# Kernel tuning notes

Measured on AMD Instinct MI355X. Metric: run time of the kernel, lower is better.

Reference implementation:

```python
import jax, jax.numpy as jnp
import numpy as np

T, H, L, OUT = 100, 100, 5, 10  # seq_len, hidden/input dim, n_lstm_layers, output dim


def _lstm_layer(x, Wih, Whh, bih, bhh):
    """Single-layer LSTM, PyTorch gate order (i, f, g, o).
    x: [T, B, H] -> outputs [T, B, H]. Zero initial state."""
    B = x.shape[1]
    b = bih + bhh  # [4H]
    # precompute input contributions for all timesteps: [T, B, 4H]
    xg = jnp.einsum('tbi,gi->tbg', x, Wih) + b

    def step(carry, xg_t):
        h, c = carry
        gates = xg_t + h @ Whh.T  # [B, 4H]
        i, f, g, o = jnp.split(gates, 4, axis=-1)
        i = jax.nn.sigmoid(i)
        f = jax.nn.sigmoid(f)
        g = jnp.tanh(g)
        o = jax.nn.sigmoid(o)
        c = f * c + i * g
        h = o * jnp.tanh(c)
        return (h, c), h

    h0 = jnp.zeros((B, H), dtype=x.dtype)
    c0 = jnp.zeros((B, H), dtype=x.dtype)
    _, ys = jax.lax.scan(step, (h0, c0), xg)
    return ys  # [T, B, H]


def setup_inputs() -> dict:
    key = jax.random.key(0)
    ks = jax.random.split(key, 7)
    s = 0.1
    return {
        'input': jax.random.normal(ks[0], (1, T, H), dtype=jnp.float32),
        'Wih': jax.random.normal(ks[1], (L, 4 * H, H), dtype=jnp.float32) * s,
        'Whh': jax.random.normal(ks[2], (L, 4 * H, H), dtype=jnp.float32) * s,
        'bih': jax.random.normal(ks[3], (L, 4 * H), dtype=jnp.float32) * s,
        'bhh': jax.random.normal(ks[4], (L, 4 * H), dtype=jnp.float32) * s,
        'W_out': jax.random.normal(ks[5], (OUT, H), dtype=jnp.float32) * s,
        'b_out': jax.random.normal(ks[6], (OUT,), dtype=jnp.float32) * s,
    }


def reference(input, Wih, Whh, bih, bhh, W_out, b_out):
    # batch_first [B, T, H] -> time-major [T, B, H] for scan
    x = jnp.transpose(input.reshape(-1, T, H), (1, 0, 2))
    for l in range(L):
        x = _lstm_layer(x, Wih[l], Whh[l], bih[l], bhh[l])
        if l < L - 1:
            x = jax.nn.relu(x)  # inter-layer ReLU (not after last LSTM)
    out = jax.nn.sigmoid(x @ W_out.T + b_out)  # [T, B, OUT]
    return jnp.transpose(out, (1, 0, 2)).reshape(T, OUT)
```

## Files before the change

kernel.cpp:

```cpp
#include <hip/hip_runtime.h>

#define TT 100
#define HH 100
#define NL 5
#define NOUT 10
#define NG 400
#define CC 10
#define NC (TT / CC)

typedef float v2f __attribute__((ext_vector_type(2)));

__device__ __forceinline__ float sigm(float x) { return 1.f / (1.f + __expf(-x)); }

#define RPT25(M) M(0) M(1) M(2) M(3) M(4) M(5) M(6) M(7) M(8) M(9) M(10) M(11) \
                 M(12) M(13) M(14) M(15) M(16) M(17) M(18) M(19) M(20) M(21) M(22) M(23) M(24)

__launch_bounds__(512, 2)
__global__ void lstm_pipe_kernel(
    const float* __restrict__ input,
    const float* __restrict__ Wih,
    const float* __restrict__ Whh,
    const float* __restrict__ bih,
    const float* __restrict__ bhh,
    const float* __restrict__ Wout,
    const float* __restrict__ bout,
    float* __restrict__ out,
    int* __restrict__ flags,
    float* __restrict__ xstage)
{
  const int l = blockIdx.x;
  const int tid = threadIdx.x;
  const int j = tid >> 2;
  const int g = tid & 3;
  const int row = g * HH + j;

  __shared__ __align__(16) float xch[CC * HH];
  __shared__ __align__(16) float och[CC * HH];
  __shared__ __align__(16) float hbuf[2][HH];

#define DECLW(k) v2f wA##k, wB##k, uA##k, uB##k;
  RPT25(DECLW)
  float bias = 0.f;
  if (tid < NG) {
    const float4* wr = (const float4*)(Wih + (size_t)l * NG * HH + (size_t)row * HH);
    const float4* ur = (const float4*)(Whh + (size_t)l * NG * HH + (size_t)row * HH);
#define LOADW(k)                                                         \
  {                                                                      \
    float4 t0 = wr[k];                                                   \
    wA##k = (v2f){t0.x, t0.y}; wB##k = (v2f){t0.z, t0.w};                \
    float4 t1 = ur[k];                                                   \
    uA##k = (v2f){t1.x, t1.y}; uB##k = (v2f){t1.z, t1.w};                \
  }
    RPT25(LOADW)
    bias = bih[l * NG + row] + bhh[l * NG + row];
  }

  float c = 0.f;
  if (tid < HH) hbuf[0][tid] = 0.f;

  for (int ch = 0; ch < NC; ++ch) {
    if (l == 0) {
      if (tid < CC * HH / 4)
        ((float4*)xch)[tid] = ((const float4*)(input + ch * CC * HH))[tid];
    } else {
      if (tid == 0) {
        const int* fl = flags + (l - 1) * NC + ch;
        while (__hip_atomic_load(fl, __ATOMIC_ACQUIRE, __HIP_MEMORY_SCOPE_AGENT) == 0)
          __builtin_amdgcn_s_sleep(1);
      }
      __syncthreads();
      const float4* src =
          (const float4*)(xstage + ((size_t)(l - 1) * TT + (size_t)ch * CC) * HH);
      if (tid < CC * HH / 4) ((float4*)xch)[tid] = src[tid];
    }

#pragma unroll 2
    for (int s = 0; s < CC; ++s) {
      __syncthreads();
      if (tid < NG) {
        const float4* h4 = (const float4*)hbuf[s & 1];
        const float4* x4 = (const float4*)(xch + s * HH);
        v2f p0 = {bias, 0.f}, p1 = {0.f, 0.f}, p2 = {0.f, 0.f}, p3 = {0.f, 0.f};
        v2f q0 = {0.f, 0.f}, q1 = {0.f, 0.f}, q2 = {0.f, 0.f}, q3 = {0.f, 0.f};
#define FMAK(k)                                                             \
  {                                                                         \
    float4 hv = h4[k];                                                      \
    float4 xv = x4[k];                                                      \
    if ((k) & 1) {                                                          \
      p0 = uA##k * (v2f){hv.x, hv.y} + p0;                                  \
      p1 = uB##k * (v2f){hv.z, hv.w} + p1;                                  \
      p2 = wA##k * (v2f){xv.x, xv.y} + p2;                                  \
      p3 = wB##k * (v2f){xv.z, xv.w} + p3;                                  \
    } else {                                                                \
      q0 = uA##k * (v2f){hv.x, hv.y} + q0;                                  \
      q1 = uB##k * (v2f){hv.z, hv.w} + q1;                                  \
      q2 = wA##k * (v2f){xv.x, xv.y} + q2;                                  \
      q3 = wB##k * (v2f){xv.z, xv.w} + q3;                                  \
    }                                                                       \
  }
        RPT25(FMAK)
        v2f tsum = ((p0 + p1) + (p2 + p3)) + ((q0 + q1) + (q2 + q3));
        float a = tsum.x + tsum.y;

        bool isg = (g == 2);
        float m = isg ? 2.f : 1.f;
        float sg = 1.f / (1.f + __expf(-m * a));
        float v = isg ? 2.f * sg - 1.f : sg;

        float v1 = __shfl_xor(v, 1);
        float v2v = __shfl_xor(v, 2);
        float v3 = __shfl_xor(v1, 2);
        if (g == 0) {
          c = v1 * c + v * v2v;
          float tc = 2.f / (1.f + __expf(-2.f * c)) - 1.f;
          float h = v3 * tc;
          hbuf[(s + 1) & 1][j] = h;
          och[s * HH + j] = (l < NL - 1) ? fmaxf(h, 0.f) : h;
        }
      }
    }
    __syncthreads();

    if (l < NL - 1) {
      float4* dst = (float4*)(xstage + ((size_t)l * TT + (size_t)ch * CC) * HH);
      if (tid < CC * HH / 4) dst[tid] = ((const float4*)och)[tid];
      __syncthreads();
      if (tid == 0) {
        __threadfence();
        __hip_atomic_store(flags + l * NC + ch, 1, __ATOMIC_RELEASE,
                           __HIP_MEMORY_SCOPE_AGENT);
      }
    } else {
      if (tid < NG) {
        int p = tid >> 2, q = tid & 3;
        int s2 = p / 10, r = p % 10;
        const float* wrow = Wout + r * HH + q * 25;
        const float* hrow = och + s2 * HH + q * 25;
        float acc = 0.f;
#pragma unroll
        for (int m2 = 0; m2 < 25; ++m2) acc = fmaf(wrow[m2], hrow[m2], acc);
        acc += __shfl_xor(acc, 1);
        acc += __shfl_xor(acc, 2);
        if (q == 0) out[(ch * CC + s2) * NOUT + r] = sigm(acc + bout[r]);
      }
    }
  }
}

extern "C" void kernel_launch(void* const* d_in, const int* in_sizes, int n_in,
                              void* d_out, int out_size, void* d_ws, size_t ws_size,
                              hipStream_t stream) {
  const float* input = (const float*)d_in[0];
  const float* Wih   = (const float*)d_in[1];
  const float* Whh   = (const float*)d_in[2];
  const float* bih   = (const float*)d_in[3];
  const float* bhh   = (const float*)d_in[4];
  const float* Wout  = (const float*)d_in[5];
  const float* bout  = (const float*)d_in[6];
  float* out = (float*)d_out;

  int* flags = (int*)d_ws;
  float* xstage = (float*)((char*)d_ws + 2048);

  hipMemsetAsync(d_ws, 0, 2048, stream);

  lstm_pipe_kernel<<<dim3(NL), dim3(512), 0, stream>>>(
      input, Wih, Whh, bih, bhh, Wout, bout, out, flags, xstage);
}
```

Before: 207.6 us.

## Switch LSTM recurrence to fp16 dot2 with pre-packed weights streamed from memory

Adds a pre-pass kernel that converts Wih/Whh to packed fp16 in a gate-interleaved layout. The recurrent kernel now streams these weights from global memory/L2 each step instead of holding them in registers, and computes gates with v_dot2_f32_f16. Activations, hidden state and the inter-layer staging buffer are also stored as fp16. This halves the FMA instruction count and the staging traffic, but each step now reloads weights from cache instead of registers, adds an extra kernel launch, and loses precision in h, x and the weights.

```diff
diff --git a/kernel.cpp b/kernel.cpp
--- a/kernel.cpp
+++ b/kernel.cpp
@@ -7,61 +7,99 @@
 #define NG 400
 #define CC 10
 #define NC (TT / CC)
-
-typedef float v2f __attribute__((ext_vector_type(2)));
+#define KC 13
+#define KH 104
+
+typedef _Float16 h2f __attribute__((ext_vector_type(2)));
 
 __device__ __forceinline__ float sigm(float x) { return 1.f / (1.f + __expf(-x)); }
 
-#define RPT25(M) M(0) M(1) M(2) M(3) M(4) M(5) M(6) M(7) M(8) M(9) M(10) M(11) \
-                 M(12) M(13) M(14) M(15) M(16) M(17) M(18) M(19) M(20) M(21) M(22) M(23) M(24)
+__device__ __forceinline__ float fdot2u(unsigned a, unsigned b, float c) {
+#if __has_builtin(__builtin_amdgcn_fdot2)
+  return __builtin_amdgcn_fdot2(__builtin_bit_cast(h2f, a),
+                                __builtin_bit_cast(h2f, b), c, false);
+#else
+  float d;
+  asm("v_dot2_f32_f16 %0, %1, %2, %3" : "=v"(d) : "v"(a), "v"(b), "v"(c));
+  return d;
+#endif
+}
+
+__device__ __forceinline__ unsigned pk16(float lo, float hi) {
+  _Float16 l = (_Float16)lo, h = (_Float16)hi;
+  return (unsigned)__builtin_bit_cast(unsigned short, l) |
+         ((unsigned)__builtin_bit_cast(unsigned short, h) << 16);
+}
+
+__global__ void pack_w(const float* __restrict__ Wih, const float* __restrict__ Whh,
+                       uint4* __restrict__ wil, uint4* __restrict__ whl) {
+  const int b = blockIdx.x;
+  const int l = b / KC, m = b % KC;
+  const int tid = threadIdx.x;
+  if (tid >= NG) return;
+  const int row = (tid & 3) * HH + (tid >> 2);
+  const float* sh = Whh + ((size_t)l * NG + row) * HH;
+  const float* si = Wih + ((size_t)l * NG + row) * HH;
+  float4 ha, hb4, ia, ib;
+  if (m < 12) {
+    ha = *(const float4*)(sh + 8 * m); hb4 = *(const float4*)(sh + 8 * m + 4);
+    ia = *(const float4*)(si + 8 * m); ib = *(const float4*)(si + 8 * m + 4);
+  } else {
+    ha = *(const float4*)(sh + 96); hb4 = make_float4(0.f, 0.f, 0.f, 0.f);
+    ia = *(const float4*)(si + 96); ib = make_float4(0.f, 0.f, 0.f, 0.f);
+  }
+  uint4 uh, ui;
+  uh.x = pk16(ha.x, ha.y); uh.y = pk16(ha.z, ha.w);
+  uh.z = pk16(hb4.x, hb4.y); uh.w = pk16(hb4.z, hb4.w);
+  ui.x = pk16(ia.x, ia.y); ui.y = pk16(ia.z, ia.w);
+  ui.z = pk16(ib.x, ib.y); ui.w = pk16(ib.z, ib.w);
+  whl[(size_t)b * NG + tid] = uh;
+  wil[(size_t)b * NG + tid] = ui;
+}
 
 __launch_bounds__(512, 2)
 __global__ void lstm_pipe_kernel(
     const float* __restrict__ input,
-    const float* __restrict__ Wih,
-    const float* __restrict__ Whh,
     const float* __restrict__ bih,
     const float* __restrict__ bhh,
     const float* __restrict__ Wout,
     const float* __restrict__ bout,
     float* __restrict__ out,
     int* __restrict__ flags,
-    float* __restrict__ xstage)
+    unsigned short* __restrict__ xst,
+    const uint4* __restrict__ whl,
+    const uint4* __restrict__ wil)
 {
+  __shared__ __align__(16) unsigned short xh[CC * KH];
+  __shared__ __align__(16) unsigned short hb[2 * KH];
+  __shared__ __align__(16) unsigned short och16[CC * KH];
+  __shared__ __align__(16) float ochf[CC * HH];
+
   const int l = blockIdx.x;
   const int tid = threadIdx.x;
   const int j = tid >> 2;
   const int g = tid & 3;
-  const int row = g * HH + j;
-
-  __shared__ __align__(16) float xch[CC * HH];
-  __shared__ __align__(16) float och[CC * HH];
-  __shared__ __align__(16) float hbuf[2][HH];
-
-#define DECLW(k) v2f wA##k, wB##k, uA##k, uB##k;
-  RPT25(DECLW)
-  float bias = 0.f;
-  if (tid < NG) {
-    const float4* wr = (const float4*)(Wih + (size_t)l * NG * HH + (size_t)row * HH);
-    const float4* ur = (const float4*)(Whh + (size_t)l * NG * HH + (size_t)row * HH);
-#define LOADW(k)                                                         \
-  {                                                                      \
-    float4 t0 = wr[k];                                                   \
-    wA##k = (v2f){t0.x, t0.y}; wB##k = (v2f){t0.z, t0.w};                \
-    float4 t1 = ur[k];                                                   \
-    uA##k = (v2f){t1.x, t1.y}; uB##k = (v2f){t1.z, t1.w};                \
-  }
-    RPT25(LOADW)
-    bias = bih[l * NG + row] + bhh[l * NG + row];
-  }
-
+  const bool act = (tid < NG);
+  const int row = act ? (g * HH + j) : 0;
+
+  const uint4* wh0 = whl + (size_t)l * KC * NG + tid;
+  const uint4* wi0 = wil + (size_t)l * KC * NG + tid;
+  const float bias = bih[l * NG + row] + bhh[l * NG + row];
+
+  if (tid < KH) { hb[tid] = 0; hb[KH + tid] = 0; }
+  if (tid < CC) {
+    *(uint2*)(xh + tid * KH + HH) = make_uint2(0u, 0u);
+    *(uint2*)(och16 + tid * KH + HH) = make_uint2(0u, 0u);
+  }
   float c = 0.f;
-  if (tid < HH) hbuf[0][tid] = 0.f;
 
   for (int ch = 0; ch < NC; ++ch) {
     if (l == 0) {
-      if (tid < CC * HH / 4)
-        ((float4*)xch)[tid] = ((const float4*)(input + ch * CC * HH))[tid];
+      if (tid < 250) {
+        float4 v = ((const float4*)(input + ch * CC * HH))[tid];
+        int s = tid / 25, q = tid % 25;
+        *(uint2*)(xh + s * KH + q * 4) = make_uint2(pk16(v.x, v.y), pk16(v.z, v.w));
+      }
     } else {
       if (tid == 0) {
         const int* fl = flags + (l - 1) * NC + ch;
@@ -69,61 +107,62 @@
           __builtin_amdgcn_s_sleep(1);
       }
       __syncthreads();
-      const float4* src =
-          (const float4*)(xstage + ((size_t)(l - 1) * TT + (size_t)ch * CC) * HH);
-      if (tid < CC * HH / 4) ((float4*)xch)[tid] = src[tid];
+      const uint4* src =
+          (const uint4*)(xst + ((size_t)(l - 1) * TT + (size_t)ch * CC) * KH);
+      if (tid < 130) ((uint4*)xh)[tid] = src[tid];
     }
 
+#define DOT(m)                                                       \
+  {                                                                  \
+    uint4 hv = hb4[m];                                               \
+    uint4 xv = xp4[m];                                               \
+    uint4 uw = wh0[(m)*NG];                                          \
+    uint4 vw = wi0[(m)*NG];                                          \
+    a0 = fdot2u(uw.x, hv.x, a0); a1 = fdot2u(uw.y, hv.y, a1);        \
+    a2 = fdot2u(uw.z, hv.z, a2); a3 = fdot2u(uw.w, hv.w, a3);        \
+    b0 = fdot2u(vw.x, xv.x, b0); b1 = fdot2u(vw.y, xv.y, b1);        \
+    b2 = fdot2u(vw.z, xv.z, b2); b3 = fdot2u(vw.w, xv.w, b3);        \
+  }
 #pragma unroll 2
     for (int s = 0; s < CC; ++s) {
       __syncthreads();
-      if (tid < NG) {
-        const float4* h4 = (const float4*)hbuf[s & 1];
-        const float4* x4 = (const float4*)(xch + s * HH);
-        v2f p0 = {bias, 0.f}, p1 = {0.f, 0.f}, p2 = {0.f, 0.f}, p3 = {0.f, 0.f};
-        v2f q0 = {0.f, 0.f}, q1 = {0.f, 0.f}, q2 = {0.f, 0.f}, q3 = {0.f, 0.f};
-#define FMAK(k)                                                             \
-  {                                                                         \
-    float4 hv = h4[k];                                                      \
-    float4 xv = x4[k];                                                      \
-    if ((k) & 1) {                                                          \
-      p0 = uA##k * (v2f){hv.x, hv.y} + p0;                                  \
-      p1 = uB##k * (v2f){hv.z, hv.w} + p1;                                  \
-      p2 = wA##k * (v2f){xv.x, xv.y} + p2;                                  \
-      p3 = wB##k * (v2f){xv.z, xv.w} + p3;                                  \
-    } else {                                                                \
-      q0 = uA##k * (v2f){hv.x, hv.y} + q0;                                  \
-      q1 = uB##k * (v2f){hv.z, hv.w} + q1;                                  \
-      q2 = wA##k * (v2f){xv.x, xv.y} + q2;                                  \
-      q3 = wB##k * (v2f){xv.z, xv.w} + q3;                                  \
-    }                                                                       \
-  }
-        RPT25(FMAK)
-        v2f tsum = ((p0 + p1) + (p2 + p3)) + ((q0 + q1) + (q2 + q3));
-        float a = tsum.x + tsum.y;
+      if (act) {
+        const uint4* hb4 = (const uint4*)(hb + (s & 1) * KH);
+        const uint4* xp4 = (const uint4*)(xh + s * KH);
+        float a0 = 0.f, a1 = 0.f, a2 = 0.f, a3 = 0.f;
+        float b0 = 0.f, b1 = 0.f, b2 = 0.f, b3 = 0.f;
+        DOT(0) DOT(1) DOT(2) DOT(3) DOT(4) DOT(5) DOT(6)
+        DOT(7) DOT(8) DOT(9) DOT(10) DOT(11) DOT(12)
+        float aa = ((a0 + a1) + (a2 + a3)) + ((b0 + b1) + (b2 + b3)) + bias;
 
         bool isg = (g == 2);
-        float m = isg ? 2.f : 1.f;
-        float sg = 1.f / (1.f + __expf(-m * a));
-        float v = isg ? 2.f * sg - 1.f : sg;
-
-        float v1 = __shfl_xor(v, 1);
-        float v2v = __shfl_xor(v, 2);
+        float mm = isg ? 2.f : 1.f;
+        float sg = 1.f / (1.f + __expf(-mm * aa));
+        float vv = isg ? 2.f * sg - 1.f : sg;
+
+        float v1 = __shfl_xor(vv, 1);
+        float v2v = __shfl_xor(vv, 2);
         float v3 = __shfl_xor(v1, 2);
         if (g == 0) {
-          c = v1 * c + v * v2v;
+          c = v1 * c + vv * v2v;
           float tc = 2.f / (1.f + __expf(-2.f * c)) - 1.f;
           float h = v3 * tc;
-          hbuf[(s + 1) & 1][j] = h;
-          och[s * HH + j] = (l < NL - 1) ? fmaxf(h, 0.f) : h;
+          hb[((s + 1) & 1) * KH + j] =
+              __builtin_bit_cast(unsigned short, (_Float16)h);
+          if (l < NL - 1) {
+            och16[s * KH + j] =
+                __builtin_bit_cast(unsigned short, (_Float16)fmaxf(h, 0.f));
+          } else {
+            ochf[s * HH + j] = h;
+          }
         }
       }
     }
     __syncthreads();
 
     if (l < NL - 1) {
-      float4* dst = (float4*)(xstage + ((size_t)l * TT + (size_t)ch * CC) * HH);
-      if (tid < CC * HH / 4) dst[tid] = ((const float4*)och)[tid];
+      uint4* dst = (uint4*)(xst + ((size_t)l * TT + (size_t)ch * CC) * KH);
+      if (tid < 130) dst[tid] = ((const uint4*)och16)[tid];
       __syncthreads();
       if (tid == 0) {
         __threadfence();
@@ -135,7 +174,7 @@
         int p = tid >> 2, q = tid & 3;
         int s2 = p / 10, r = p % 10;
         const float* wrow = Wout + r * HH + q * 25;
-        const float* hrow = och + s2 * HH + q * 25;
+        const float* hrow = ochf + s2 * HH + q * 25;
         float acc = 0.f;
 #pragma unroll
         for (int m2 = 0; m2 < 25; ++m2) acc = fmaf(wrow[m2], hrow[m2], acc);
@@ -160,10 +199,14 @@
   float* out = (float*)d_out;
 
   int* flags = (int*)d_ws;
-  float* xstage = (float*)((char*)d_ws + 2048);
+  unsigned short* xst = (unsigned short*)((char*)d_ws + 2048);
+  uint4* whl = (uint4*)((char*)d_ws + 85248);
+  uint4* wil = (uint4*)((char*)d_ws + 501248);
 
   hipMemsetAsync(d_ws, 0, 2048, stream);
 
+  pack_w<<<dim3(NL * KC), dim3(512), 0, stream>>>(Wih, Whh, wil, whl);
+
   lstm_pipe_kernel<<<dim3(NL), dim3(512), 0, stream>>>(
-      input, Wih, Whh, bih, bhh, Wout, bout, out, flags, xstage);
-}
+      input, bih, bhh, Wout, bout, out, flags, xst, whl, wil);
+}
```

Result: slower. 296.5 us (+42.8%).

## Switch LSTM recurrence to fp16 dot2 with weights held in AGPRs

Applied to the files above, without the earlier changes.

Weights are converted to packed fp16 and kept in accumulation registers. Each thread now computes all four gates for one hidden unit over a quarter of the reduction dimension, using v_dot2_f32_f16 and a DPP quad reduction in place of per-gate threads and shuffles. Inter-layer activations are staged as fp16 in a padded layout, and a separate pre-kernel packs the input for layer 0. This targets fewer instructions and less LDS/global traffic on the serial per-step path, at the cost of reduced precision in the weights and hidden state plus an extra kernel launch.

```diff
diff --git a/kernel.cpp b/kernel.cpp
--- a/kernel.cpp
+++ b/kernel.cpp
@@ -4,20 +4,64 @@
 #define HH 100
 #define NL 5
 #define NOUT 10
-#define NG 400
 #define CC 10
 #define NC (TT / CC)
-
-typedef float v2f __attribute__((ext_vector_type(2)));
+#define RW 64
+#define NTH 448
+
+typedef _Float16 h2f __attribute__((ext_vector_type(2)));
 
 __device__ __forceinline__ float sigm(float x) { return 1.f / (1.f + __expf(-x)); }
 
-#define RPT25(M) M(0) M(1) M(2) M(3) M(4) M(5) M(6) M(7) M(8) M(9) M(10) M(11) \
-                 M(12) M(13) M(14) M(15) M(16) M(17) M(18) M(19) M(20) M(21) M(22) M(23) M(24)
-
-__launch_bounds__(512, 2)
-__global__ void lstm_pipe_kernel(
-    const float* __restrict__ input,
+__device__ __forceinline__ float fdot2u(unsigned a, unsigned b, float c) {
+#if __has_builtin(__builtin_amdgcn_fdot2)
+  return __builtin_amdgcn_fdot2(__builtin_bit_cast(h2f, a),
+                                __builtin_bit_cast(h2f, b), c, false);
+#else
+  float d;
+  asm("v_dot2_f32_f16 %0, %1, %2, %3" : "=v"(d) : "v"(a), "v"(b), "v"(c));
+  return d;
+#endif
+}
+
+__device__ __forceinline__ unsigned pk16(float lo, float hi) {
+  _Float16 l = (_Float16)lo, h = (_Float16)hi;
+  return (unsigned)__builtin_bit_cast(unsigned short, l) |
+         ((unsigned)__builtin_bit_cast(unsigned short, h) << 16);
+}
+
+__device__ __forceinline__ float qred(float p) {
+  int t = __builtin_amdgcn_update_dpp(0, __builtin_bit_cast(int, p), 0xB1, 0xF,
+                                      0xF, true);
+  p += __builtin_bit_cast(float, t);
+  t = __builtin_amdgcn_update_dpp(0, __builtin_bit_cast(int, p), 0x4E, 0xF, 0xF,
+                                  true);
+  p += __builtin_bit_cast(float, t);
+  return p;
+}
+
+#define R13(M) M(0) M(1) M(2) M(3) M(4) M(5) M(6) M(7) M(8) M(9) M(10) M(11) M(12)
+
+#define AWR(D, S) asm volatile("v_accvgpr_write_b32 %0, %1" : "=a"(D) : "v"(S));
+#define ARD(D, S) asm("v_accvgpr_read_b32 %0, %1" : "=v"(D) : "a"(S));
+
+__global__ void pack_x0(const float* __restrict__ in, unsigned* __restrict__ x0) {
+  for (int idx = blockIdx.x * 512 + threadIdx.x; idx < TT * RW;
+       idx += gridDim.x * 512) {
+    int t = idx / RW, d = idx & (RW - 1);
+    int q = d >> 4, m = d & 15;
+    unsigned v = 0u;
+    int k0 = 26 * q + 2 * m;
+    if (m < 13 && k0 < 100) {
+      v = pk16(in[t * HH + k0], in[t * HH + k0 + 1]);
+    }
+    x0[idx] = v;
+  }
+}
+
+__global__ __attribute__((amdgpu_flat_work_group_size(NTH, NTH),
+                          amdgpu_waves_per_eu(2, 2)))
+void lstm_pipe_kernel(
     const float* __restrict__ Wih,
     const float* __restrict__ Whh,
     const float* __restrict__ bih,
@@ -26,104 +70,152 @@
     const float* __restrict__ bout,
     float* __restrict__ out,
     int* __restrict__ flags,
-    float* __restrict__ xstage)
+    unsigned* __restrict__ xst)
 {
+  __shared__ __align__(16) unsigned xh32[CC * RW];
+  __shared__ __align__(16) unsigned och32[CC * RW];
+  __shared__ __align__(16) unsigned hb32[2 * RW];
+  __shared__ __align__(16) float ochf[CC * HH];
+
   const int l = blockIdx.x;
   const int tid = threadIdx.x;
   const int j = tid >> 2;
-  const int g = tid & 3;
-  const int row = g * HH + j;
-
-  __shared__ __align__(16) float xch[CC * HH];
-  __shared__ __align__(16) float och[CC * HH];
-  __shared__ __align__(16) float hbuf[2][HH];
-
-#define DECLW(k) v2f wA##k, wB##k, uA##k, uB##k;
-  RPT25(DECLW)
-  float bias = 0.f;
-  if (tid < NG) {
-    const float4* wr = (const float4*)(Wih + (size_t)l * NG * HH + (size_t)row * HH);
-    const float4* ur = (const float4*)(Whh + (size_t)l * NG * HH + (size_t)row * HH);
-#define LOADW(k)                                                         \
-  {                                                                      \
-    float4 t0 = wr[k];                                                   \
-    wA##k = (v2f){t0.x, t0.y}; wB##k = (v2f){t0.z, t0.w};                \
-    float4 t1 = ur[k];                                                   \
-    uA##k = (v2f){t1.x, t1.y}; uB##k = (v2f){t1.z, t1.w};                \
+  const int q = tid & 3;
+  const bool act = (tid < 400);
+  const int hwpos = (j / 26) * 32 + (j % 26);
+
+#define DECLM(m) unsigned H0_##m, H1_##m, H2_##m, H3_##m, \
+                          I0_##m, I1_##m, I2_##m, I3_##m;
+  R13(DECLM)
+
+  float b0 = 0.f, b1 = 0.f, b2 = 0.f, b3 = 0.f;
+  if (act) {
+    const int kq = 26 * q;
+    const float* ph0 = Whh + (size_t)(l * 400 + 0 * 100 + j) * 100 + kq;
+    const float* ph1 = Whh + (size_t)(l * 400 + 1 * 100 + j) * 100 + kq;
+    const float* ph2 = Whh + (size_t)(l * 400 + 2 * 100 + j) * 100 + kq;
+    const float* ph3 = Whh + (size_t)(l * 400 + 3 * 100 + j) * 100 + kq;
+    const float* pi0 = Wih + (size_t)(l * 400 + 0 * 100 + j) * 100 + kq;
+    const float* pi1 = Wih + (size_t)(l * 400 + 1 * 100 + j) * 100 + kq;
+    const float* pi2 = Wih + (size_t)(l * 400 + 2 * 100 + j) * 100 + kq;
+    const float* pi3 = Wih + (size_t)(l * 400 + 3 * 100 + j) * 100 + kq;
+#define LDM(m)                                                           \
+    {                                                                    \
+      const bool ok = (kq + 2 * (m)) < 100;                              \
+      float2 f; unsigned u;                                              \
+      f = ok ? *(const float2*)(ph0 + 2 * (m)) : make_float2(0.f, 0.f);  \
+      u = pk16(f.x, f.y); AWR(H0_##m, u)                                 \
+      f = ok ? *(const float2*)(ph1 + 2 * (m)) : make_float2(0.f, 0.f);  \
+      u = pk16(f.x, f.y); AWR(H1_##m, u)                                 \
+      f = ok ? *(const float2*)(ph2 + 2 * (m)) : make_float2(0.f, 0.f);  \
+      u = pk16(f.x, f.y); AWR(H2_##m, u)                                 \
+      f = ok ? *(const float2*)(ph3 + 2 * (m)) : make_float2(0.f, 0.f);  \
+      u = pk16(f.x, f.y); AWR(H3_##m, u)                                 \
+      f = ok ? *(const float2*)(pi0 + 2 * (m)) : make_float2(0.f, 0.f);  \
+      u = pk16(f.x, f.y); AWR(I0_##m, u)                                 \
+      f = ok ? *(const float2*)(pi1 + 2 * (m)) : make_float2(0.f, 0.f);  \
+      u = pk16(f.x, f.y); AWR(I1_##m, u)                                 \
+      f = ok ? *(const float2*)(pi2 + 2 * (m)) : make_float2(0.f, 0.f);  \
+      u = pk16(f.x, f.y); AWR(I2_##m, u)                                 \
+      f = ok ? *(const float2*)(pi3 + 2 * (m)) : make_float2(0.f, 0.f);  \
+      u = pk16(f.x, f.y); AWR(I3_##m, u)                                 \
+    }
+    R13(LDM)
+    if (q == 0) {
+      b0 = bih[l * 400 + 0 * 100 + j] + bhh[l * 400 + 0 * 100 + j];
+      b1 = bih[l * 400 + 1 * 100 + j] + bhh[l * 400 + 1 * 100 + j];
+      b2 = bih[l * 400 + 2 * 100 + j] + bhh[l * 400 + 2 * 100 + j];
+      b3 = bih[l * 400 + 3 * 100 + j] + bhh[l * 400 + 3 * 100 + j];
+    }
   }
-    RPT25(LOADW)
-    bias = bih[l * NG + row] + bhh[l * NG + row];
-  }
-
+
+  if (tid < 2 * RW) hb32[tid] = 0u;
+  if (tid < 160) ((uint4*)och32)[tid] = make_uint4(0u, 0u, 0u, 0u);
   float c = 0.f;
-  if (tid < HH) hbuf[0][tid] = 0.f;
+  __syncthreads();
 
   for (int ch = 0; ch < NC; ++ch) {
-    if (l == 0) {
-      if (tid < CC * HH / 4)
-        ((float4*)xch)[tid] = ((const float4*)(input + ch * CC * HH))[tid];
-    } else {
+    if (l > 0) {
       if (tid == 0) {
         const int* fl = flags + (l - 1) * NC + ch;
         while (__hip_atomic_load(fl, __ATOMIC_ACQUIRE, __HIP_MEMORY_SCOPE_AGENT) == 0)
           __builtin_amdgcn_s_sleep(1);
       }
       __syncthreads();
-      const float4* src =
-          (const float4*)(xstage + ((size_t)(l - 1) * TT + (size_t)ch * CC) * HH);
-      if (tid < CC * HH / 4) ((float4*)xch)[tid] = src[tid];
-    }
-
-#pragma unroll 2
-    for (int s = 0; s < CC; ++s) {
-      __syncthreads();
-      if (tid < NG) {
-        const float4* h4 = (const float4*)hbuf[s & 1];
-        const float4* x4 = (const float4*)(xch + s * HH);
-        v2f p0 = {bias, 0.f}, p1 = {0.f, 0.f}, p2 = {0.f, 0.f}, p3 = {0.f, 0.f};
-        v2f q0 = {0.f, 0.f}, q1 = {0.f, 0.f}, q2 = {0.f, 0.f}, q3 = {0.f, 0.f};
-#define FMAK(k)                                                             \
-  {                                                                         \
-    float4 hv = h4[k];                                                      \
-    float4 xv = x4[k];                                                      \
-    if ((k) & 1) {                                                          \
-      p0 = uA##k * (v2f){hv.x, hv.y} + p0;                                  \
-      p1 = uB##k * (v2f){hv.z, hv.w} + p1;                                  \
-      p2 = wA##k * (v2f){xv.x, xv.y} + p2;                                  \
-      p3 = wB##k * (v2f){xv.z, xv.w} + p3;                                  \
-    } else {                                                                \
-      q0 = uA##k * (v2f){hv.x, hv.y} + q0;                                  \
-      q1 = uB##k * (v2f){hv.z, hv.w} + q1;                                  \
-      q2 = wA##k * (v2f){xv.x, xv.y} + q2;                                  \
-      q3 = wB##k * (v2f){xv.z, xv.w} + q3;                                  \
-    }                                                                       \
-  }
-        RPT25(FMAK)
-        v2f tsum = ((p0 + p1) + (p2 + p3)) + ((q0 + q1) + (q2 + q3));
-        float a = tsum.x + tsum.y;
-
-        bool isg = (g == 2);
-        float m = isg ? 2.f : 1.f;
-        float sg = 1.f / (1.f + __expf(-m * a));
-        float v = isg ? 2.f * sg - 1.f : sg;
-
-        float v1 = __shfl_xor(v, 1);
-        float v2v = __shfl_xor(v, 2);
-        float v3 = __shfl_xor(v1, 2);
-        if (g == 0) {
-          c = v1 * c + v * v2v;
-          float tc = 2.f / (1.f + __expf(-2.f * c)) - 1.f;
-          float h = v3 * tc;
-          hbuf[(s + 1) & 1][j] = h;
-          och[s * HH + j] = (l < NL - 1) ? fmaxf(h, 0.f) : h;
-        }
-      }
-    }
+    }
+    {
+      const uint4* src = (const uint4*)(xst + ((size_t)l * TT + ch * CC) * RW);
+      if (tid < 160) ((uint4*)xh32)[tid] = src[tid];
+    }
+
+#define GPART(gg, P)                                     \
+    {                                                    \
+      unsigned w; float p = 0.f, px = 0.f;               \
+      ARD(w, H##gg##_0)  p = fdot2u(w, ha.x, p);         \
+      ARD(w, H##gg##_1)  p = fdot2u(w, ha.y, p);         \
+      ARD(w, H##gg##_2)  p = fdot2u(w, ha.z, p);         \
+      ARD(w, H##gg##_3)  p = fdot2u(w, ha.w, p);         \
+      ARD(w, H##gg##_4)  p = fdot2u(w, hbv.x, p);        \
+      ARD(w, H##gg##_5)  p = fdot2u(w, hbv.y, p);        \
+      ARD(w, H##gg##_6)  p = fdot2u(w, hbv.z, p);        \
+      ARD(w, H##gg##_7)  p = fdot2u(w, hbv.w, p);        \
+      ARD(w, H##gg##_8)  p = fdot2u(w, hcv.x, p);        \
+      ARD(w, H##gg##_9)  p = fdot2u(w, hcv.y, p);        \
+      ARD(w, H##gg##_10) p = fdot2u(w, hcv.z, p);        \
+      ARD(w, H##gg##_11) p = fdot2u(w, hcv.w, p);        \
+      ARD(w, H##gg##_12) p = fdot2u(w, hd, p);           \
+      ARD(w, I##gg##_0)  px = fdot2u(w, xa.x, px);       \
+      ARD(w, I##gg##_1)  px = fdot2u(w, xa.y, px);       \
+      ARD(w, I##gg##_2)  px = fdot2u(w, xa.z, px);       \
+      ARD(w, I##gg##_3)  px = fdot2u(w, xa.w, px);       \
+      ARD(w, I##gg##_4)  px = fdot2u(w, xbv.x, px);      \
+      ARD(w, I##gg##_5)  px = fdot2u(w, xbv.y, px);      \
+      ARD(w, I##gg##_6)  px = fdot2u(w, xbv.z, px);      \
+      ARD(w, I##gg##_7)  px = fdot2u(w, xbv.w, px);      \
+      ARD(w, I##gg##_8)  px = fdot2u(w, xcv.x, px);      \
+      ARD(w, I##gg##_9)  px = fdot2u(w, xcv.y, px);      \
+      ARD(w, I##gg##_10) px = fdot2u(w, xcv.z, px);      \
+      ARD(w, I##gg##_11) px = fdot2u(w, xcv.w, px);      \
+      ARD(w, I##gg##_12) px = fdot2u(w, xd, px);         \
+      P = p + px;                                        \
+    }
+#define STEP(s)                                                               \
+    {                                                                         \
+      __syncthreads();                \
+      if (act) {                                                              \
+        const uint4* hp = (const uint4*)(hb32 + (((s) & 1) << 6) + (q << 4)); \
+        const uint4* xp = (const uint4*)(xh32 + ((s) << 6) + (q << 4));       \
+        uint4 ha = hp[0], hbv = hp[1], hcv = hp[2];                           \
+        unsigned hd = ((const unsigned*)hp)[12];                              \
+        uint4 xa = xp[0], xbv = xp[1], xcv = xp[2];                           \
+        unsigned xd = ((const unsigned*)xp)[12];                              \
+        float P0, P1, P2, P3;                                                 \
+        GPART(0, P0) GPART(1, P1) GPART(2, P2) GPART(3, P3)                   \
+        P0 = qred(P0); P1 = qred(P1); P2 = qred(P2); P3 = qred(P3);           \
+        if (q == 0) {                                                         \
+          float gi = sigm(P0 + b0), gf = sigm(P1 + b1);                       \
+          float gv = 2.f * sigm(2.f * (P2 + b2)) - 1.f;                       \
+          float go = sigm(P3 + b3);                                           \
+          c = gf * c + gi * gv;                                               \
+          float h = go * (2.f * sigm(2.f * c) - 1.f);                         \
+          ((unsigned short*)hb32)[((((s) + 1) & 1) << 7) + hwpos] =           \
+              __builtin_bit_cast(unsigned short, (_Float16)h);                \
+          if (l < NL - 1)                                                     \
+            ((unsigned short*)och32)[((s) << 7) + hwpos] =                    \
+                __builtin_bit_cast(unsigned short, (_Float16)fmaxf(h, 0.f));  \
+          else                                                                \
+            ochf[(s) * HH + j] = h;                                           \
+        }                                                                     \
+      }                                                                       \
+    }
+    STEP(0) STEP(1) STEP(2) STEP(3) STEP(4)
+    STEP(5) STEP(6) STEP(7) STEP(8) STEP(9)
+
     __syncthreads();
 
     if (l < NL - 1) {
-      float4* dst = (float4*)(xstage + ((size_t)l * TT + (size_t)ch * CC) * HH);
-      if (tid < CC * HH / 4) dst[tid] = ((const float4*)och)[tid];
+      uint4* dst = (uint4*)(xst + ((size_t)(l + 1) * TT + ch * CC) * RW);
+      if (tid < 160) dst[tid] = ((const uint4*)och32)[tid];
       __syncthreads();
       if (tid == 0) {
         __threadfence();
@@ -131,16 +223,14 @@
                            __HIP_MEMORY_SCOPE_AGENT);
       }
     } else {
-      if (tid < NG) {
-        int p = tid >> 2, q = tid & 3;
-        int s2 = p / 10, r = p % 10;
+      if (act) {
+        int s2 = j / 10, r = j % 10;
         const float* wrow = Wout + r * HH + q * 25;
-        const float* hrow = och + s2 * HH + q * 25;
+        const float* hrow = ochf + s2 * HH + q * 25;
         float acc = 0.f;
 #pragma unroll
         for (int m2 = 0; m2 < 25; ++m2) acc = fmaf(wrow[m2], hrow[m2], acc);
-        acc += __shfl_xor(acc, 1);
-        acc += __shfl_xor(acc, 2);
+        acc = qred(acc);
         if (q == 0) out[(ch * CC + s2) * NOUT + r] = sigm(acc + bout[r]);
       }
     }
@@ -160,10 +250,12 @@
   float* out = (float*)d_out;
 
   int* flags = (int*)d_ws;
-  float* xstage = (float*)((char*)d_ws + 2048);
+  unsigned* xst = (unsigned*)((char*)d_ws + 2048);
 
   hipMemsetAsync(d_ws, 0, 2048, stream);
 
-  lstm_pipe_kernel<<<dim3(NL), dim3(512), 0, stream>>>(
-      input, Wih, Whh, bih, bhh, Wout, bout, out, flags, xstage);
-}
+  pack_x0<<<dim3(4), dim3(512), 0, stream>>>(input, xst);
+
+  lstm_pipe_kernel<<<dim3(NL), dim3(NTH), 0, stream>>>(
+      Wih, Whh, bih, bhh, Wout, bout, out, flags, xst);
+}
```

Result: slower. 232.0 us (+11.7%).

## Move LSTM gate matmuls to split-fp16 MFMA with per-chunk input projection

Applied to the files above, without the earlier changes.

Replaces the per-thread fp32 FMA dot products with v_mfma_f32_16x16x32_f16 matrix instructions. Operands are split into hi/lo fp16 pairs to keep roughly fp32 accuracy. The input projection for each 10-step chunk is now computed in one batch of MFMAs, leaving only the recurrent Whh product on the serial path, with gate math done by 100 threads after a shared-memory exchange. Inter-layer activations are staged as packed hi/lo fp16, and a small pre-kernel packs the first layer's input. The cost is extra MFMAs (mostly wasted columns), hand-inserted nops, two barriers per step and one more kernel launch.

```diff
diff --git a/kernel.cpp b/kernel.cpp
--- a/kernel.cpp
+++ b/kernel.cpp
@@ -4,20 +4,81 @@
 #define HH 100
 #define NL 5
 #define NOUT 10
-#define NG 400
 #define CC 10
 #define NC (TT / CC)
-
-typedef float v2f __attribute__((ext_vector_type(2)));
+#define XROW 128
+#define XR2 256
+#define TPB 512
+
+typedef _Float16 f16x8 __attribute__((ext_vector_type(8)));
+typedef float f32x4 __attribute__((ext_vector_type(4)));
 
 __device__ __forceinline__ float sigm(float x) { return 1.f / (1.f + __expf(-x)); }
 
-#define RPT25(M) M(0) M(1) M(2) M(3) M(4) M(5) M(6) M(7) M(8) M(9) M(10) M(11) \
-                 M(12) M(13) M(14) M(15) M(16) M(17) M(18) M(19) M(20) M(21) M(22) M(23) M(24)
-
-__launch_bounds__(512, 2)
-__global__ void lstm_pipe_kernel(
-    const float* __restrict__ input,
+__device__ __forceinline__ float qred(float p) {
+  int t = __builtin_amdgcn_update_dpp(0, __builtin_bit_cast(int, p), 0xB1, 0xF,
+                                      0xF, true);
+  p += __builtin_bit_cast(float, t);
+  t = __builtin_amdgcn_update_dpp(0, __builtin_bit_cast(int, p), 0x4E, 0xF, 0xF,
+                                  true);
+  p += __builtin_bit_cast(float, t);
+  return p;
+}
+
+#define MFA(ACC, A, B)                                                   \
+  asm volatile("s_nop 2\n\tv_mfma_f32_16x16x32_f16 %0, %1, %2, %0"       \
+               : "+v"(ACC) : "a"(A), "v"(B));
+#define MFV(ACC, A, B)                                                   \
+  asm volatile("s_nop 2\n\tv_mfma_f32_16x16x32_f16 %0, %1, %2, %0"       \
+               : "+v"(ACC) : "v"(A), "v"(B));
+#define NOPV(X) asm volatile("s_nop 7\n\ts_nop 7\n\ts_nop 2" : "+v"(X));
+
+#define FR16(M)                                                         \
+  M(0, 0) M(0, 1) M(0, 2) M(0, 3) M(1, 0) M(1, 1) M(1, 2) M(1, 3)       \
+  M(2, 0) M(2, 1) M(2, 2) M(2, 3) M(3, 0) M(3, 1) M(3, 2) M(3, 3)
+
+struct fragpair { f16x8 hi, lo; };
+
+__device__ __forceinline__ fragpair ldfrag2(const float* base, int r, int kb) {
+  f16x8 h, l;
+#pragma unroll
+  for (int e = 0; e < 8; ++e) {
+    float v = 0.f;
+    if (r < 400 && (kb + e) < 100) v = base[r * 100 + kb + e];
+    _Float16 vh = (_Float16)v;
+    h[e] = vh;
+    l[e] = (_Float16)(v - (float)vh);
+  }
+  fragpair fp; fp.hi = h; fp.lo = l;
+  return fp;
+}
+
+__device__ __forceinline__ f16x8 bcf(uint4 u) { return __builtin_bit_cast(f16x8, u); }
+
+__device__ __forceinline__ unsigned pk2(_Float16 lo, _Float16 hi) {
+  return (unsigned)__builtin_bit_cast(unsigned short, lo) |
+         ((unsigned)__builtin_bit_cast(unsigned short, hi) << 16);
+}
+
+__global__ void pack_x0(const float* __restrict__ in, unsigned* __restrict__ x0) {
+  for (int idx = blockIdx.x * 512 + threadIdx.x; idx < TT * (XR2 / 2);
+       idx += gridDim.x * 512) {
+    int t = idx >> 7, d = idx & 127;
+    int k0 = 2 * (d & 63);
+    unsigned v = 0u;
+    if (k0 < 100) {
+      float a = in[t * HH + k0], b = in[t * HH + k0 + 1];
+      _Float16 ah = (_Float16)a, bh = (_Float16)b;
+      if (d < 64) v = pk2(ah, bh);
+      else v = pk2((_Float16)(a - (float)ah), (_Float16)(b - (float)bh));
+    }
+    x0[idx] = v;
+  }
+}
+
+__global__ __attribute__((amdgpu_flat_work_group_size(TPB, TPB),
+                          amdgpu_waves_per_eu(2, 2)))
+void lstm_pipe_kernel(
     const float* __restrict__ Wih,
     const float* __restrict__ Whh,
     const float* __restrict__ bih,
@@ -26,104 +87,159 @@
     const float* __restrict__ bout,
     float* __restrict__ out,
     int* __restrict__ flags,
-    float* __restrict__ xstage)
+    unsigned short* __restrict__ xst)
 {
+  __shared__ __align__(16) unsigned short xch[CC * XR2];
+  __shared__ __align__(16) unsigned short och16[CC * XR2];
+  __shared__ __align__(16) unsigned short hbuf[2 * XR2];
+  __shared__ __align__(16) float gsumS[512];
+  __shared__ __align__(16) float gsumL[512];
+  __shared__ __align__(16) float ochf[CC * HH];
+
   const int l = blockIdx.x;
   const int tid = threadIdx.x;
-  const int j = tid >> 2;
-  const int g = tid & 3;
-  const int row = g * HH + j;
-
-  __shared__ __align__(16) float xch[CC * HH];
-  __shared__ __align__(16) float och[CC * HH];
-  __shared__ __align__(16) float hbuf[2][HH];
-
-#define DECLW(k) v2f wA##k, wB##k, uA##k, uB##k;
-  RPT25(DECLW)
-  float bias = 0.f;
-  if (tid < NG) {
-    const float4* wr = (const float4*)(Wih + (size_t)l * NG * HH + (size_t)row * HH);
-    const float4* ur = (const float4*)(Whh + (size_t)l * NG * HH + (size_t)row * HH);
-#define LOADW(k)                                                         \
-  {                                                                      \
-    float4 t0 = wr[k];                                                   \
-    wA##k = (v2f){t0.x, t0.y}; wB##k = (v2f){t0.z, t0.w};                \
-    float4 t1 = ur[k];                                                   \
-    uA##k = (v2f){t1.x, t1.y}; uB##k = (v2f){t1.z, t1.w};                \
-  }
-    RPT25(LOADW)
-    bias = bih[l * NG + row] + bhh[l * NG + row];
-  }
-
-  float c = 0.f;
-  if (tid < HH) hbuf[0][tid] = 0.f;
+  const int lane = tid & 63;
+  const int w4 = (tid >> 6) * 4;
+  const int row16 = lane & 15;
+  const int col = lane & 15;
+  const int kg8 = (lane >> 4) << 3;
+  const int kg4 = (lane >> 4) << 2;
+
+  const float* WhhL = Whh + (size_t)l * 40000;
+  const float* WihL = Wih + (size_t)l * 40000;
+
+#define DW(t, k) f16x8 WHH##t##k, WHL##t##k;
+  FR16(DW)
+#define LDW(t, k)                                                          \
+  { fragpair fp_ = ldfrag2(WhhL, (w4 + (t)) * 16 + row16, (k) * 32 + kg8); \
+    WHH##t##k = fp_.hi; WHL##t##k = fp_.lo; }
+  FR16(LDW)
+
+  float bi0 = 0.f, bi1 = 0.f, bi2 = 0.f, bi3 = 0.f, cc_ = 0.f;
+  if (tid < HH) {
+    bi0 = bih[l * 400 + tid] + bhh[l * 400 + tid];
+    bi1 = bih[l * 400 + 100 + tid] + bhh[l * 400 + 100 + tid];
+    bi2 = bih[l * 400 + 200 + tid] + bhh[l * 400 + 200 + tid];
+    bi3 = bih[l * 400 + 300 + tid] + bhh[l * 400 + 300 + tid];
+  }
+  if (tid < 64) ((uint4*)hbuf)[tid] = make_uint4(0u, 0u, 0u, 0u);
+  if (tid < 320) ((uint4*)och16)[tid] = make_uint4(0u, 0u, 0u, 0u);
+  __syncthreads();
 
   for (int ch = 0; ch < NC; ++ch) {
-    if (l == 0) {
-      if (tid < CC * HH / 4)
-        ((float4*)xch)[tid] = ((const float4*)(input + ch * CC * HH))[tid];
-    } else {
+    if (l > 0) {
       if (tid == 0) {
         const int* fl = flags + (l - 1) * NC + ch;
         while (__hip_atomic_load(fl, __ATOMIC_ACQUIRE, __HIP_MEMORY_SCOPE_AGENT) == 0)
           __builtin_amdgcn_s_sleep(1);
       }
       __syncthreads();
-      const float4* src =
-          (const float4*)(xstage + ((size_t)(l - 1) * TT + (size_t)ch * CC) * HH);
-      if (tid < CC * HH / 4) ((float4*)xch)[tid] = src[tid];
-    }
-
-#pragma unroll 2
-    for (int s = 0; s < CC; ++s) {
-      __syncthreads();
-      if (tid < NG) {
-        const float4* h4 = (const float4*)hbuf[s & 1];
-        const float4* x4 = (const float4*)(xch + s * HH);
-        v2f p0 = {bias, 0.f}, p1 = {0.f, 0.f}, p2 = {0.f, 0.f}, p3 = {0.f, 0.f};
-        v2f q0 = {0.f, 0.f}, q1 = {0.f, 0.f}, q2 = {0.f, 0.f}, q3 = {0.f, 0.f};
-#define FMAK(k)                                                             \
-  {                                                                         \
-    float4 hv = h4[k];                                                      \
-    float4 xv = x4[k];                                                      \
-    if ((k) & 1) {                                                          \
-      p0 = uA##k * (v2f){hv.x, hv.y} + p0;                                  \
-      p1 = uB##k * (v2f){hv.z, hv.w} + p1;                                  \
-      p2 = wA##k * (v2f){xv.x, xv.y} + p2;                                  \
-      p3 = wB##k * (v2f){xv.z, xv.w} + p3;                                  \
-    } else {                                                                \
-      q0 = uA##k * (v2f){hv.x, hv.y} + q0;                                  \
-      q1 = uB##k * (v2f){hv.z, hv.w} + q1;                                  \
-      q2 = wA##k * (v2f){xv.x, xv.y} + q2;                                  \
-      q3 = wB##k * (v2f){xv.z, xv.w} + q3;                                  \
-    }                                                                       \
-  }
-        RPT25(FMAK)
-        v2f tsum = ((p0 + p1) + (p2 + p3)) + ((q0 + q1) + (q2 + q3));
-        float a = tsum.x + tsum.y;
-
-        bool isg = (g == 2);
-        float m = isg ? 2.f : 1.f;
-        float sg = 1.f / (1.f + __expf(-m * a));
-        float v = isg ? 2.f * sg - 1.f : sg;
-
-        float v1 = __shfl_xor(v, 1);
-        float v2v = __shfl_xor(v, 2);
-        float v3 = __shfl_xor(v1, 2);
-        if (g == 0) {
-          c = v1 * c + v * v2v;
-          float tc = 2.f / (1.f + __expf(-2.f * c)) - 1.f;
-          float h = v3 * tc;
-          hbuf[(s + 1) & 1][j] = h;
-          och[s * HH + j] = (l < NL - 1) ? fmaxf(h, 0.f) : h;
-        }
-      }
+    }
+    {
+      const uint4* src = (const uint4*)(xst + ((size_t)l * TT + ch * CC) * XR2);
+      if (tid < 320) ((uint4*)xch)[tid] = src[tid];
     }
     __syncthreads();
 
+    f32x4 XA0 = {0.f, 0.f, 0.f, 0.f}, XA1 = {0.f, 0.f, 0.f, 0.f};
+    f32x4 XA2 = {0.f, 0.f, 0.f, 0.f}, XA3 = {0.f, 0.f, 0.f, 0.f};
+    {
+      uint4 z4 = make_uint4(0u, 0u, 0u, 0u);
+      uint4 u0 = z4, u1 = z4, u2 = z4, u3 = z4;
+      uint4 v0 = z4, v1 = z4, v2 = z4, v3 = z4;
+      if (col < CC) {
+        const unsigned short* xph = xch + col * XR2 + kg8;
+        const unsigned short* xpl = xph + XROW;
+        u0 = *(const uint4*)(xph + 0);  u1 = *(const uint4*)(xph + 32);
+        u2 = *(const uint4*)(xph + 64); u3 = *(const uint4*)(xph + 96);
+        v0 = *(const uint4*)(xpl + 0);  v1 = *(const uint4*)(xpl + 32);
+        v2 = *(const uint4*)(xpl + 64); v3 = *(const uint4*)(xpl + 96);
+      }
+      f16x8 Xh0 = bcf(u0), Xh1 = bcf(u1), Xh2 = bcf(u2), Xh3 = bcf(u3);
+      f16x8 Xl0 = bcf(v0), Xl1 = bcf(v1), Xl2 = bcf(v2), Xl3 = bcf(v3);
+#define XAT(t)                                                           \
+      if (w4 + (t) < 25) {                                               \
+        const int rr = (w4 + (t)) * 16 + row16;                          \
+        fragpair f0 = ldfrag2(WihL, rr, 0 + kg8);                        \
+        fragpair f1 = ldfrag2(WihL, rr, 32 + kg8);                       \
+        fragpair f2 = ldfrag2(WihL, rr, 64 + kg8);                       \
+        fragpair f3 = ldfrag2(WihL, rr, 96 + kg8);                       \
+        MFV(XA##t, f0.hi, Xh0) MFV(XA##t, f1.hi, Xh1)                    \
+        MFV(XA##t, f2.hi, Xh2) MFV(XA##t, f3.hi, Xh3)                    \
+        MFV(XA##t, f0.lo, Xh0) MFV(XA##t, f1.lo, Xh1)                    \
+        MFV(XA##t, f2.lo, Xh2) MFV(XA##t, f3.lo, Xh3)                    \
+        MFV(XA##t, f0.hi, Xl0) MFV(XA##t, f1.hi, Xl1)                    \
+        MFV(XA##t, f2.hi, Xl2) MFV(XA##t, f3.hi, Xl3)                    \
+        MFV(XA##t, f0.lo, Xl0) MFV(XA##t, f1.lo, Xl1)                    \
+        MFV(XA##t, f2.lo, Xl2) MFV(XA##t, f3.lo, Xl3)                    \
+        NOPV(XA##t)                                                      \
+      }
+      XAT(0) XAT(1) XAT(2) XAT(3)
+    }
+
+#define TILEC(t, s, LCv)                                                 \
+      if (w4 + (t) < 25) {                                               \
+        f32x4 dd = XA##t;                                                \
+        MFA(dd, WHH##t##0, fB0) MFA(dd, WHH##t##1, fB1)                  \
+        MFA(dd, WHH##t##2, fB2) MFA(dd, WHH##t##3, fB3)                  \
+        MFA(dd, WHL##t##0, fB0) MFA(dd, WHL##t##1, fB1)                  \
+        MFA(dd, WHL##t##2, fB2) MFA(dd, WHL##t##3, fB3)                  \
+        NOPV(dd)                                                         \
+        const int rbt = (w4 + (t)) * 16 + kg4;                           \
+        if (col == (s)) *(f32x4*)(gsumS + rbt) = dd;                     \
+        else if (col == (LCv)) *(f32x4*)(gsumL + rbt) = dd;              \
+      }
+#define STEP(s)                                                               \
+    {                                                                         \
+      const int p = (s) & 1;                                                  \
+      const int LCv = 10 + ((s) % 6);                                         \
+      const unsigned short* hph = hbuf + p * XR2 + kg8;                       \
+      const unsigned short* hpl = hph + XROW;                                 \
+      uint4 z4s = make_uint4(0u, 0u, 0u, 0u);                                 \
+      uint4 q0 = z4s, q1 = z4s, q2 = z4s, q3 = z4s;                           \
+      if (col == (s)) {                                                       \
+        q0 = *(const uint4*)(hph + 0);  q1 = *(const uint4*)(hph + 32);       \
+        q2 = *(const uint4*)(hph + 64); q3 = *(const uint4*)(hph + 96);       \
+      } else if (col == LCv) {                                                \
+        q0 = *(const uint4*)(hpl + 0);  q1 = *(const uint4*)(hpl + 32);       \
+        q2 = *(const uint4*)(hpl + 64); q3 = *(const uint4*)(hpl + 96);       \
+      }                                                                       \
+      f16x8 fB0 = bcf(q0), fB1 = bcf(q1), fB2 = bcf(q2), fB3 = bcf(q3);       \
+      TILEC(0, s, LCv) TILEC(1, s, LCv) TILEC(2, s, LCv) TILEC(3, s, LCv)     \
+      __syncthreads();                                     \
+      if (tid < HH) {                                                         \
+        float s0 = gsumS[tid] + gsumL[tid] + bi0;                             \
+        float s1 = gsumS[100 + tid] + gsumL[100 + tid] + bi1;                 \
+        float s2 = gsumS[200 + tid] + gsumL[200 + tid] + bi2;                 \
+        float s3 = gsumS[300 + tid] + gsumL[300 + tid] + bi3;                 \
+        float gi = sigm(s0), gf = sigm(s1);                                   \
+        float gv = 2.f * sigm(2.f * s2) - 1.f, go = sigm(s3);                 \
+        cc_ = gf * cc_ + gi * gv;                                             \
+        float h = go * (2.f * sigm(2.f * cc_) - 1.f);                         \
+        _Float16 hhi = (_Float16)h;                                           \
+        _Float16 hlo = (_Float16)(h - (float)hhi);                            \
+        hbuf[(p ^ 1) * XR2 + tid] = __builtin_bit_cast(unsigned short, hhi);  \
+        hbuf[(p ^ 1) * XR2 + XROW + tid] =                                    \
+            __builtin_bit_cast(unsigned short, hlo);                          \
+        if (l < NL - 1) {                                                     \
+          float hr = fmaxf(h, 0.f);                                           \
+          _Float16 rhi = (_Float16)hr;                                        \
+          _Float16 rlo = (_Float16)(hr - (float)rhi);                         \
+          och16[(s) * XR2 + tid] = __builtin_bit_cast(unsigned short, rhi);   \
+          och16[(s) * XR2 + XROW + tid] =                                     \
+              __builtin_bit_cast(unsigned short, rlo);                        \
+        } else {                                                              \
+          ochf[(s) * HH + tid] = h;                                           \
+        }                                                                     \
+      }                                                                       \
+      __syncthreads();                            \
+    }
+    STEP(0) STEP(1) STEP(2) STEP(3) STEP(4)
+    STEP(5) STEP(6) STEP(7) STEP(8) STEP(9)
+
     if (l < NL - 1) {
-      float4* dst = (float4*)(xstage + ((size_t)l * TT + (size_t)ch * CC) * HH);
-      if (tid < CC * HH / 4) dst[tid] = ((const float4*)och)[tid];
+      uint4* dst = (uint4*)(xst + ((size_t)(l + 1) * TT + ch * CC) * XR2);
+      if (tid < 320) dst[tid] = ((const uint4*)och16)[tid];
       __syncthreads();
       if (tid == 0) {
         __threadfence();
@@ -131,18 +247,18 @@
                            __HIP_MEMORY_SCOPE_AGENT);
       }
     } else {
-      if (tid < NG) {
-        int p = tid >> 2, q = tid & 3;
-        int s2 = p / 10, r = p % 10;
+      if (tid < 400) {
+        int j = tid >> 2, q = tid & 3;
+        int s2 = j / 10, r = j % 10;
         const float* wrow = Wout + r * HH + q * 25;
-        const float* hrow = och + s2 * HH + q * 25;
+        const float* hrow = ochf + s2 * HH + q * 25;
         float acc = 0.f;
 #pragma unroll
         for (int m2 = 0; m2 < 25; ++m2) acc = fmaf(wrow[m2], hrow[m2], acc);
-        acc += __shfl_xor(acc, 1);
-        acc += __shfl_xor(acc, 2);
+        acc = qred(acc);
         if (q == 0) out[(ch * CC + s2) * NOUT + r] = sigm(acc + bout[r]);
       }
+      __syncthreads();
     }
   }
 }
@@ -160,10 +276,12 @@
   float* out = (float*)d_out;
 
   int* flags = (int*)d_ws;
-  float* xstage = (float*)((char*)d_ws + 2048);
+  unsigned short* xst = (unsigned short*)((char*)d_ws + 2048);
 
   hipMemsetAsync(d_ws, 0, 2048, stream);
 
-  lstm_pipe_kernel<<<dim3(NL), dim3(512), 0, stream>>>(
-      input, Wih, Whh, bih, bhh, Wout, bout, out, flags, xstage);
-}
+  pack_x0<<<dim3(8), dim3(512), 0, stream>>>(input, (unsigned*)xst);
+
+  lstm_pipe_kernel<<<dim3(NL), dim3(TPB), 0, stream>>>(
+      Wih, Whh, bih, bhh, Wout, bout, out, flags, xst);
+}
```

Result: slower. 306.9 us (+47.8%).
